# Optimization experiments

Measured on AMD Instinct MI355X. Metric: run time of the kernel, lower is better.

## Reference

```python
import jax, jax.numpy as jnp
import numpy as np

N_HEADS = 16

def setup_inputs() -> dict:
    key = jax.random.key(0)
    qkv = jax.random.normal(key, (4, 3072, 2048), dtype=jnp.float32)
    return {"qkv": qkv}

def reference(qkv) -> jnp.ndarray:
    bs, width, length = qkv.shape
    ch = width // (3 * N_HEADS)
    # [bs*H, 3*ch, T] -> split into q, k, v each [bs*H, ch, T]
    qkv_r = qkv.reshape(bs * N_HEADS, 3 * ch, length)
    q, k, v = qkv_r[:, :ch], qkv_r[:, ch:2 * ch], qkv_r[:, 2 * ch:]
    scale = 1.0 / jnp.sqrt(jnp.sqrt(jnp.float32(ch)))
    # scores: [bs*H, T, T]
    weight = jnp.einsum('bct,bcs->bts', q * scale, k * scale)
    weight = jax.nn.softmax(weight.astype(jnp.float32), axis=-1).astype(weight.dtype)
    a = jnp.einsum('bts,bcs->bct', weight, v)  # [bs*H, ch, T]
    return a.reshape(bs, N_HEADS * ch, length)
```

## Files before the change

### kernel.cpp

```cpp
#include <hip/hip_runtime.h>

namespace {

constexpr int D  = 64;
constexpr int T  = 2048;
constexpr int NT = T / 64;
constexpr float SCL = 0.125f * 1.44269504088896340736f;

constexpr size_t QP_OFF  = (size_t)64 * 32 * 8192;
constexpr size_t WS_NEED = ((size_t)64 * 32 * 8192 + (size_t)64 * 32 * 4096) * 2;

typedef __bf16 bf16x8 __attribute__((ext_vector_type(8)));
typedef float  f32x4  __attribute__((ext_vector_type(4)));
typedef unsigned short u16x4 __attribute__((ext_vector_type(4)));
typedef unsigned short u16x8 __attribute__((ext_vector_type(8)));
typedef unsigned int   u32x2 __attribute__((ext_vector_type(2)));
typedef short          s16x4 __attribute__((ext_vector_type(4)));

__device__ inline unsigned short f2bf(float f) {
    unsigned int u = __builtin_bit_cast(unsigned int, f);
    u += 0x7FFFu + ((u >> 16) & 1u);
    return (unsigned short)(u >> 16);
}

__device__ inline unsigned int pkbf(float a, float b) {
#if __has_builtin(__builtin_amdgcn_cvt_pk_bf16_f32)
    auto r = __builtin_amdgcn_cvt_pk_bf16_f32(a, b);
    static_assert(sizeof(r) == 4, "cvt_pk_bf16 size");
    return __builtin_bit_cast(unsigned int, r);
#else
    return (unsigned int)f2bf(a) | ((unsigned int)f2bf(b) << 16);
#endif
}

__device__ inline int frag_off(int row, int c0) {
    int g = (c0 >> 3) ^ ((row >> 1) & 7);
    return row * 64 + g * 8;
}

__device__ inline void async_cp16(const void* g, void* l) {
    __builtin_amdgcn_global_load_lds(
        (const __attribute__((address_space(1))) unsigned int*)g,
        (__attribute__((address_space(3))) unsigned int*)l, 16, 0, 0);
}

__global__ __launch_bounds__(256)
void prepass(const float* __restrict__ qkv, unsigned short* __restrict__ ws) {
    const int tile = blockIdx.x, h = blockIdx.y, z = blockIdx.z;
    const int tid = threadIdx.x;
    const float* src = qkv + (size_t)h * 3 * D * T + (size_t)z * D * T + tile * 64;
    __shared__ unsigned short L[4096];

    if (z == 2) {
        unsigned short* dst = ws + (size_t)(h * 32 + tile) * 8192 + 4096;
        const int c = tid >> 2, g = tid & 3;
        const int sg = g ^ ((c >> 2) & 3);
        #pragma unroll
        for (int wq = 0; wq < 4; wq++) {
            f32x4 a = *(const f32x4*)(src + (size_t)c * T + wq * 16 + sg * 4);
            u16x4 wv = { f2bf(a[0]), f2bf(a[1]), f2bf(a[2]), f2bf(a[3]) };
            *(u16x4*)(dst + wq * 1024 + tid * 4) = wv;
        }
    } else {
        const float m = (z == 0) ? SCL : 1.0f;
        const int c0 = (tid >> 4) * 4, s4 = tid & 15;
        float fr[4][4];
        #pragma unroll
        for (int r = 0; r < 4; r++)
            *(f32x4*)fr[r] = *(const f32x4*)(src + (size_t)(c0 + r) * T + s4 * 4);
        #pragma unroll
        for (int j = 0; j < 4; j++) {
            int trow = s4 * 4 + j;
            u16x4 wv = { f2bf(fr[0][j] * m), f2bf(fr[1][j] * m),
                         f2bf(fr[2][j] * m), f2bf(fr[3][j] * m) };
            *(u16x4*)(L + frag_off(trow, c0) + (c0 & 7)) = wv;
        }
        __syncthreads();
        unsigned short* dst = (z == 0)
            ? ws + QP_OFF + (size_t)(h * 32 + tile) * 4096
            : ws + (size_t)(h * 32 + tile) * 8192;
        #pragma unroll
        for (int i = 0; i < 2; i++)
            *(u16x8*)(dst + tid * 16 + i * 8) = *(const u16x8*)(L + tid * 16 + i * 8);
    }
}


#define STAGE(J, SB)                                                         \
  { const char* g = kvb + (size_t)(J) * 16384;                               \
    char* lk = lbase + (SB) * 16384;                                         \
    async_cp16(g,         lk);                                               \
    async_cp16(g + 4096,  lk + 4096);                                        \
    async_cp16(g + 8192,  lk + 8192);                                        \
    async_cp16(g + 12288, lk + 12288); }

#define BODY(KT, B, SB, DO_STAGE, WAITIMM)                                   \
  {                                                                          \
    __builtin_amdgcn_s_waitcnt(WAITIMM);         \
    __builtin_amdgcn_s_barrier();                    \
    __builtin_amdgcn_sched_barrier(0);          \
    if (DO_STAGE) STAGE((KT) + 2, SB)     \
    __builtin_amdgcn_s_setprio(1);                                           \
    _Pragma("unroll")                                                        \
    for (int qq = 0; qq < 4; qq++) {                                         \
      const char* kb = sbuf + (B) * 16384 + qq * 2048;                       \
      const char* vb = sbuf + (B) * 16384 + 8192 + qq * 2048;                \
      bf16x8 aK0 = *(const bf16x8*)(kb + aK0o);                              \
      bf16x8 aK1 = *(const bf16x8*)(kb + aK1o);                              \
      s16x4 aV0 = *(const s16x4*)(vb + aVo);                                 \
      s16x4 aV1 = *(const s16x4*)(vb + aVo + 512);                           \
      s16x4 aV2 = *(const s16x4*)(vb + aVo + 1024);                          \
      s16x4 aV3 = *(const s16x4*)(vb + aVo + 1536);                          \
      _Pragma("unroll")                                                      \
      for (int st = 0; st < 2; st++) {                                       \
        f32x4 s = __builtin_amdgcn_mfma_f32_16x16x32_bf16(                   \
            aK0, bQ[st][0], ZF, 0, 0, 0);                                    \
        s = __builtin_amdgcn_mfma_f32_16x16x32_bf16(aK1, bQ[st][1], s, 0,0,0);\
        float p0 = __builtin_amdgcn_exp2f(s[0]);                             \
        float p1 = __builtin_amdgcn_exp2f(s[1]);                             \
        float p2 = __builtin_amdgcn_exp2f(s[2]);                             \
        float p3 = __builtin_amdgcn_exp2f(s[3]);                             \
        l_acc[st] += (p0 + p1) + (p2 + p3);                                  \
        u32x2 pk = { pkbf(p0, p1), pkbf(p2, p3) };                           \
        s16x4 bP = __builtin_bit_cast(s16x4, pk);                            \
        acc_o[st][0] = __builtin_amdgcn_mfma_f32_16x16x16bf16_1k(            \
            aV0, bP, acc_o[st][0], 0, 0, 0);                                 \
        acc_o[st][1] = __builtin_amdgcn_mfma_f32_16x16x16bf16_1k(            \
            aV1, bP, acc_o[st][1], 0, 0, 0);                                 \
        acc_o[st][2] = __builtin_amdgcn_mfma_f32_16x16x16bf16_1k(            \
            aV2, bP, acc_o[st][2], 0, 0, 0);                                 \
        acc_o[st][3] = __builtin_amdgcn_mfma_f32_16x16x16bf16_1k(            \
            aV3, bP, acc_o[st][3], 0, 0, 0);                                 \
      }                                                                      \
    }                                                                        \
    __builtin_amdgcn_s_setprio(0);                                           \
  }

__global__ __launch_bounds__(256, 3)
void attn_main(const unsigned short* __restrict__ ws, float* __restrict__ out) {
    const int h  = blockIdx.x;
    const int qt = blockIdx.y;
    const int t0 = qt * 128;
    const int tid  = threadIdx.x;
    const int lane = tid & 63;
    const int w    = tid >> 6;
    const int ln   = lane & 15, q4 = lane >> 4;

    __shared__ char sbuf[49152];
    char* lbase = sbuf + w * 1024;

    const int aK0o = 2 * frag_off(ln, q4 * 8);
    const int aK1o = 2 * frag_off(ln, 32 + q4 * 8);
    const int aVo  = 32 * ln + 2 * ((q4 ^ ((ln >> 2) & 3)) * 4);

    const unsigned short* qtile = ws + QP_OFF + (size_t)(h * 32 + qt * 2) * 4096;
    bf16x8 bQ[2][2];
    #pragma unroll
    for (int st = 0; st < 2; st++) {
        bQ[st][0] = *(const bf16x8*)(qtile + st * 4096 + frag_off(16 * w + ln, q4 * 8));
        bQ[st][1] = *(const bf16x8*)(qtile + st * 4096 + frag_off(16 * w + ln, 32 + q4 * 8));
    }

    const char* kvb = (const char*)ws + (size_t)(h * 32) * 16384
                      + w * 1024 + lane * 16;
    STAGE(0, 0)
    STAGE(1, 1)

    const f32x4 ZF = {0.f, 0.f, 0.f, 0.f};
    f32x4 acc_o[2][4];
    #pragma unroll
    for (int st = 0; st < 2; st++)
        #pragma unroll
        for (int ci = 0; ci < 4; ci++) acc_o[st][ci] = ZF;
    float l_acc[2] = {0.f, 0.f};

    #pragma unroll 1
    for (int m = 0; m < 10; m++) {
        BODY(3 * m,     0, 2, 1, 0x0F74)
        BODY(3 * m + 1, 1, 0, 1, 0x0F74)
        BODY(3 * m + 2, 2, 1, 1, 0x0F74)
    }
    BODY(30, 0, 0, 0, 0x0F74)
    BODY(31, 1, 0, 0, 0x0F70)

    #pragma unroll
    for (int st = 0; st < 2; st++) {
        float sl = l_acc[st];
        sl += __shfl_xor(sl, 16, 64);
        sl += __shfl_xor(sl, 32, 64);
        const float linv = 1.0f / sl;
        float* ob = out + (size_t)h * D * T + t0 + st * 64 + 16 * w + ln;
        #pragma unroll
        for (int ci = 0; ci < 4; ci++)
            #pragma unroll
            for (int rr = 0; rr < 4; rr++)
                ob[(size_t)(16 * ci + q4 * 4 + rr) * T] = acc_o[st][ci][rr] * linv;
    }
}

__device__ inline bf16x8 frag8(const unsigned short* p, int row, int c0) {
    return *(const bf16x8*)(p + frag_off(row, c0));
}

__global__ __launch_bounds__(256)
void attn_fallback(const float* __restrict__ qkv, float* __restrict__ out) {
    const int h     = blockIdx.y;
    const int t0    = blockIdx.x * 64;
    const int tid   = threadIdx.x;
    const int lane  = tid & 63;
    const int strip = tid >> 6;
    const int ln    = lane & 15;
    const int q4    = lane >> 4;

    __shared__ unsigned short Qs[64 * D];
    __shared__ unsigned short Ks[64 * D];
    __shared__ unsigned short Vs[D * 64];
    __shared__ unsigned short Pss[64 * 64];
    __shared__ float l_lds[64];

    const float* qb = qkv + (size_t)h * 3 * D * T;
    const float* kb = qb + (size_t)D * T;
    const float* vb = qb + (size_t)(2 * D) * T;
    const int s4 = tid & 15;
    const int c0 = (tid >> 4) * 4;
    {
        float fr[4][4];
        #pragma unroll
        for (int r = 0; r < 4; r++)
            *(f32x4*)fr[r] = *(const f32x4*)(qb + (size_t)(c0 + r) * T + t0 + s4 * 4);
        #pragma unroll
        for (int j = 0; j < 4; j++) {
            int trow = s4 * 4 + j;
            u16x4 wv = { f2bf(fr[0][j]), f2bf(fr[1][j]), f2bf(fr[2][j]), f2bf(fr[3][j]) };
            *(u16x4*)(Qs + frag_off(trow, c0) + (c0 & 7)) = wv;
        }
    }
    __syncthreads();
    const int arow = strip * 16 + ln;
    const int kg   = q4 * 8;
    const bf16x8 aq0 = frag8(Qs, arow, kg);
    const bf16x8 aq1 = frag8(Qs, arow, 32 + kg);
    f32x4 acc_o[4];
    #pragma unroll
    for (int m = 0; m < 4; m++) acc_o[m] = (f32x4){0.f, 0.f, 0.f, 0.f};
    float l_acc[4] = {0.f, 0.f, 0.f, 0.f};
    constexpr float S2 = 0.125f * 1.44269504088896340736f;
    for (int kt = 0; kt < NT; kt++) {
        const int s0 = kt * 64;
        float kr[4][4], vr[4][4];
        #pragma unroll
        for (int r = 0; r < 4; r++)
            *(f32x4*)kr[r] = *(const f32x4*)(kb + (size_t)(c0 + r) * T + s0 + s4 * 4);
        #pragma unroll
        for (int r = 0; r < 4; r++)
            *(f32x4*)vr[r] = *(const f32x4*)(vb + (size_t)(c0 + r) * T + s0 + s4 * 4);
        __syncthreads();
        #pragma unroll
        for (int j = 0; j < 4; j++) {
            int srow = s4 * 4 + j;
            u16x4 wk = { f2bf(kr[0][j]), f2bf(kr[1][j]), f2bf(kr[2][j]), f2bf(kr[3][j]) };
            *(u16x4*)(Ks + frag_off(srow, c0) + (c0 & 7)) = wk;
        }
        #pragma unroll
        for (int r = 0; r < 4; r++) {
            int row = c0 + r, cc = s4 * 4;
            u16x4 wv = { f2bf(vr[r][0]), f2bf(vr[r][1]), f2bf(vr[r][2]), f2bf(vr[r][3]) };
            *(u16x4*)(Vs + frag_off(row, cc) + (cc & 7)) = wv;
        }
        __syncthreads();
        f32x4 accs[4];
        #pragma unroll
        for (int ns = 0; ns < 4; ns++) {
            bf16x8 b0 = frag8(Ks, ns * 16 + ln, kg);
            bf16x8 b1 = frag8(Ks, ns * 16 + ln, 32 + kg);
            f32x4 z = {0.f, 0.f, 0.f, 0.f};
            z = __builtin_amdgcn_mfma_f32_16x16x32_bf16(aq0, b0, z, 0, 0, 0);
            z = __builtin_amdgcn_mfma_f32_16x16x32_bf16(aq1, b1, z, 0, 0, 0);
            accs[ns] = z;
        }
        #pragma unroll
        for (int ns = 0; ns < 4; ns++) {
            int scol = ns * 16 + ln;
            #pragma unroll
            for (int r = 0; r < 4; r++) {
                float p = __builtin_amdgcn_exp2f(accs[ns][r] * S2);
                l_acc[r] += p;
                int trow = strip * 16 + q4 * 4 + r;
                int g = ((scol >> 3) ^ ((trow >> 1) & 7));
                Pss[trow * 64 + g * 8 + (scol & 7)] = f2bf(p);
            }
        }
        bf16x8 bp0 = frag8(Pss, arow, kg);
        bf16x8 bp1 = frag8(Pss, arow, 32 + kg);
        #pragma unroll
        for (int ms = 0; ms < 4; ms++) {
            bf16x8 av0 = frag8(Vs, ms * 16 + ln, kg);
            bf16x8 av1 = frag8(Vs, ms * 16 + ln, 32 + kg);
            acc_o[ms] = __builtin_amdgcn_mfma_f32_16x16x32_bf16(av0, bp0, acc_o[ms], 0, 0, 0);
            acc_o[ms] = __builtin_amdgcn_mfma_f32_16x16x32_bf16(av1, bp1, acc_o[ms], 0, 0, 0);
        }
    }
    #pragma unroll
    for (int r = 0; r < 4; r++) {
        float s = l_acc[r];
        s += __shfl_xor(s, 1, 64);
        s += __shfl_xor(s, 2, 64);
        s += __shfl_xor(s, 4, 64);
        s += __shfl_xor(s, 8, 64);
        if (ln == 0) l_lds[strip * 16 + q4 * 4 + r] = s;
    }
    const float linv = 1.0f / l_lds[strip * 16 + ln];
    const int tg = t0 + strip * 16 + ln;
    float* ob = out + (size_t)h * D * T;
    #pragma unroll
    for (int ms = 0; ms < 4; ms++)
        #pragma unroll
        for (int r = 0; r < 4; r++) {
            int c = ms * 16 + q4 * 4 + r;
            ob[(size_t)c * T + tg] = acc_o[ms][r] * linv;
        }
}

}

extern "C" void kernel_launch(void* const* d_in, const int* in_sizes, int n_in,
                              void* d_out, int out_size, void* d_ws, size_t ws_size,
                              hipStream_t stream) {
    const float* qkv = (const float*)d_in[0];
    float* out = (float*)d_out;
    if (ws_size >= WS_NEED) {
        prepass<<<dim3(32, 64, 3), 256, 0, stream>>>(qkv, (unsigned short*)d_ws);
        attn_main<<<dim3(64, 16), 256, 0, stream>>>((const unsigned short*)d_ws, out);
    } else {
        attn_fallback<<<dim3(32, 64), 256, 0, stream>>>(qkv, out);
    }
}
```

Before: 251.9 us.

## Use 16x16x32 bf16 MFMA for PV by pairing key subtiles

The PV product now processes two 16-key subtiles at once, computing two score tiles and packing eight probabilities into one bf16x8 operand, so it can use the K=32 MFMA instead of two K=16 MFMAs. The V layout written by the prepass changes to match, storing 8-element fragments per lane with a new swizzle and 16-byte LDS reads. This halves the number of PV MFMA issues and LDS read instructions, but raises register pressure from the extra live K fragments and scores.

```diff
diff --git a/kernel.cpp b/kernel.cpp
--- a/kernel.cpp
+++ b/kernel.cpp
@@ -15,7 +15,7 @@
 typedef unsigned short u16x4 __attribute__((ext_vector_type(4)));
 typedef unsigned short u16x8 __attribute__((ext_vector_type(8)));
 typedef unsigned int   u32x2 __attribute__((ext_vector_type(2)));
-typedef short          s16x4 __attribute__((ext_vector_type(4)));
+typedef unsigned int   u32x4 __attribute__((ext_vector_type(4)));
 
 __device__ inline unsigned short f2bf(float f) {
     unsigned int u = __builtin_bit_cast(unsigned int, f);
@@ -53,13 +53,15 @@
 
     if (z == 2) {
         unsigned short* dst = ws + (size_t)(h * 32 + tile) * 8192 + 4096;
-        const int c = tid >> 2, g = tid & 3;
-        const int sg = g ^ ((c >> 2) & 3);
-        #pragma unroll
-        for (int wq = 0; wq < 4; wq++) {
-            f32x4 a = *(const f32x4*)(src + (size_t)c * T + wq * 16 + sg * 4);
-            u16x4 wv = { f2bf(a[0]), f2bf(a[1]), f2bf(a[2]), f2bf(a[3]) };
-            *(u16x4*)(dst + wq * 1024 + tid * 4) = wv;
+        const int c = tid >> 2, pg = tid & 3;
+        const int slot = pg ^ ((c >> 2) & 3);
+        #pragma unroll
+        for (int b = 0; b < 2; b++) {
+            f32x4 a0 = *(const f32x4*)(src + (size_t)c * T + b * 32 + pg * 4);
+            f32x4 a1 = *(const f32x4*)(src + (size_t)c * T + b * 32 + 16 + pg * 4);
+            u16x8 wv = { f2bf(a0[0]), f2bf(a0[1]), f2bf(a0[2]), f2bf(a0[3]),
+                         f2bf(a1[0]), f2bf(a1[1]), f2bf(a1[2]), f2bf(a1[3]) };
+            *(u16x8*)(dst + b * 2048 + c * 32 + slot * 8) = wv;
         }
     } else {
         const float m = (z == 0) ? SCL : 1.0f;
@@ -97,40 +99,53 @@
 #define BODY(KT, B, SB, DO_STAGE, WAITIMM)                                   \
   {                                                                          \
     __builtin_amdgcn_s_waitcnt(WAITIMM);         \
-    __builtin_amdgcn_s_barrier();                    \
+    __builtin_amdgcn_s_barrier();          \
     __builtin_amdgcn_sched_barrier(0);          \
     if (DO_STAGE) STAGE((KT) + 2, SB)     \
     __builtin_amdgcn_s_setprio(1);                                           \
     _Pragma("unroll")                                                        \
-    for (int qq = 0; qq < 4; qq++) {                                         \
-      const char* kb = sbuf + (B) * 16384 + qq * 2048;                       \
-      const char* vb = sbuf + (B) * 16384 + 8192 + qq * 2048;                \
-      bf16x8 aK0 = *(const bf16x8*)(kb + aK0o);                              \
-      bf16x8 aK1 = *(const bf16x8*)(kb + aK1o);                              \
-      s16x4 aV0 = *(const s16x4*)(vb + aVo);                                 \
-      s16x4 aV1 = *(const s16x4*)(vb + aVo + 512);                           \
-      s16x4 aV2 = *(const s16x4*)(vb + aVo + 1024);                          \
-      s16x4 aV3 = *(const s16x4*)(vb + aVo + 1536);                          \
+    for (int j = 0; j < 2; j++) {         \
+      const char* kq0 = sbuf + (B) * 16384 + (2 * j) * 2048;                 \
+      const char* kq1 = kq0 + 2048;                                          \
+      const char* vbj = sbuf + (B) * 16384 + 8192 + j * 4096;                \
+      bf16x8 aK00 = *(const bf16x8*)(kq0 + aK0o);                            \
+      bf16x8 aK01 = *(const bf16x8*)(kq0 + aK1o);                            \
+      bf16x8 aK10 = *(const bf16x8*)(kq1 + aK0o);                            \
+      bf16x8 aK11 = *(const bf16x8*)(kq1 + aK1o);                            \
+      bf16x8 aV0 = *(const bf16x8*)(vbj + aVo);                              \
+      bf16x8 aV1 = *(const bf16x8*)(vbj + aVo + 1024);                       \
+      bf16x8 aV2 = *(const bf16x8*)(vbj + aVo + 2048);                       \
+      bf16x8 aV3 = *(const bf16x8*)(vbj + aVo + 3072);                       \
       _Pragma("unroll")                                                      \
       for (int st = 0; st < 2; st++) {                                       \
-        f32x4 s = __builtin_amdgcn_mfma_f32_16x16x32_bf16(                   \
-            aK0, bQ[st][0], ZF, 0, 0, 0);                                    \
-        s = __builtin_amdgcn_mfma_f32_16x16x32_bf16(aK1, bQ[st][1], s, 0,0,0);\
-        float p0 = __builtin_amdgcn_exp2f(s[0]);                             \
-        float p1 = __builtin_amdgcn_exp2f(s[1]);                             \
-        float p2 = __builtin_amdgcn_exp2f(s[2]);                             \
-        float p3 = __builtin_amdgcn_exp2f(s[3]);                             \
-        l_acc[st] += (p0 + p1) + (p2 + p3);                                  \
-        u32x2 pk = { pkbf(p0, p1), pkbf(p2, p3) };                           \
-        s16x4 bP = __builtin_bit_cast(s16x4, pk);                            \
-        acc_o[st][0] = __builtin_amdgcn_mfma_f32_16x16x16bf16_1k(            \
-            aV0, bP, acc_o[st][0], 0, 0, 0);                                 \
-        acc_o[st][1] = __builtin_amdgcn_mfma_f32_16x16x16bf16_1k(            \
-            aV1, bP, acc_o[st][1], 0, 0, 0);                                 \
-        acc_o[st][2] = __builtin_amdgcn_mfma_f32_16x16x16bf16_1k(            \
-            aV2, bP, acc_o[st][2], 0, 0, 0);                                 \
-        acc_o[st][3] = __builtin_amdgcn_mfma_f32_16x16x16bf16_1k(            \
-            aV3, bP, acc_o[st][3], 0, 0, 0);                                 \
+        f32x4 s0 = __builtin_amdgcn_mfma_f32_16x16x32_bf16(                  \
+            aK00, bQ[st][0], ZF, 0, 0, 0);                                   \
+        s0 = __builtin_amdgcn_mfma_f32_16x16x32_bf16(                        \
+            aK01, bQ[st][1], s0, 0, 0, 0);                                   \
+        f32x4 s1 = __builtin_amdgcn_mfma_f32_16x16x32_bf16(                  \
+            aK10, bQ[st][0], ZF, 0, 0, 0);                                   \
+        s1 = __builtin_amdgcn_mfma_f32_16x16x32_bf16(                        \
+            aK11, bQ[st][1], s1, 0, 0, 0);                                   \
+        float p0 = __builtin_amdgcn_exp2f(s0[0]);                            \
+        float p1 = __builtin_amdgcn_exp2f(s0[1]);                            \
+        float p2 = __builtin_amdgcn_exp2f(s0[2]);                            \
+        float p3 = __builtin_amdgcn_exp2f(s0[3]);                            \
+        float q0 = __builtin_amdgcn_exp2f(s1[0]);                            \
+        float q1 = __builtin_amdgcn_exp2f(s1[1]);                            \
+        float q2 = __builtin_amdgcn_exp2f(s1[2]);                            \
+        float q3 = __builtin_amdgcn_exp2f(s1[3]);                            \
+        l_acc[st] += ((p0 + p1) + (p2 + p3)) + ((q0 + q1) + (q2 + q3));      \
+        u32x4 pk = { pkbf(p0, p1), pkbf(p2, p3),                             \
+                     pkbf(q0, q1), pkbf(q2, q3) };                           \
+        bf16x8 bPP = __builtin_bit_cast(bf16x8, pk);                         \
+        acc_o[st][0] = __builtin_amdgcn_mfma_f32_16x16x32_bf16(              \
+            aV0, bPP, acc_o[st][0], 0, 0, 0);                                \
+        acc_o[st][1] = __builtin_amdgcn_mfma_f32_16x16x32_bf16(              \
+            aV1, bPP, acc_o[st][1], 0, 0, 0);                                \
+        acc_o[st][2] = __builtin_amdgcn_mfma_f32_16x16x32_bf16(              \
+            aV2, bPP, acc_o[st][2], 0, 0, 0);                                \
+        acc_o[st][3] = __builtin_amdgcn_mfma_f32_16x16x32_bf16(              \
+            aV3, bPP, acc_o[st][3], 0, 0, 0);                                \
       }                                                                      \
     }                                                                        \
     __builtin_amdgcn_s_setprio(0);                                           \
@@ -151,7 +166,7 @@
 
     const int aK0o = 2 * frag_off(ln, q4 * 8);
     const int aK1o = 2 * frag_off(ln, 32 + q4 * 8);
-    const int aVo  = 32 * ln + 2 * ((q4 ^ ((ln >> 2) & 3)) * 4);
+    const int aVo  = 64 * ln + ((q4 ^ ((ln >> 2) & 3)) * 16);
 
     const unsigned short* qtile = ws + QP_OFF + (size_t)(h * 32 + qt * 2) * 4096;
     bf16x8 bQ[2][2];
```

Measured after the change: 238.9 us. 1.05x faster.
